# Performance work log

Measured on AMD Instinct MI355X. Metric: run time of the kernel, lower is better.

The kernel has to match this reference:

```python
import jax, jax.numpy as jnp
import numpy as np

B, T, NG, NP, DV = 256, 100, 4096, 512, 2


def setup_inputs() -> dict:
    key = jax.random.key(0)
    k = jax.random.split(key, 6)
    v = jax.random.normal(k[0], (B, T, DV), dtype=jnp.float32) * 0.1
    P0 = jax.random.uniform(k[1], (B, NP), dtype=jnp.float32)
    # Dense kernels (glorot-ish scale); recurrent kernel uniform(-0.02, 0.02) per the module
    W_enc = jax.random.normal(k[2], (NP, NG), dtype=jnp.float32) / np.sqrt(NP)
    W_in = jax.random.normal(k[3], (DV, NG), dtype=jnp.float32) / np.sqrt(DV)
    W_rec = (jax.random.uniform(k[4], (NG, NG), dtype=jnp.float32) * 2.0 - 1.0) * 0.02
    W_dec = jax.random.normal(k[5], (NG, NP), dtype=jnp.float32) / np.sqrt(NG)
    return {"v": v, "P0": P0, "W_enc": W_enc, "W_in": W_in, "W_rec": W_rec, "W_dec": W_dec}


def reference(v, P0, W_enc, W_in, W_rec, W_dec):
    # encoder: init hidden state from place-cell code P0  -> [B, Ng]
    h0 = P0 @ W_enc
    # Precompute input projection for all timesteps: [B, T, Ng] -> scan over T
    xW = jnp.einsum('btd,dg->btg', v, W_in)
    xW_t = jnp.swapaxes(xW, 0, 1)  # [T, B, Ng]

    def step(h, x):
        h_new = jax.nn.relu(x + h @ W_rec)
        return h_new, h_new

    _, g = jax.lax.scan(step, h0, xW_t)      # g: [T, B, Ng]
    g = jnp.swapaxes(g, 0, 1)                # [B, T, Ng]
    place_preds = jnp.einsum('btg,gp->btp', g, W_dec)  # [B, T, Np]
    return place_preds
```

## Files before the change

### kernel.cpp

```cpp
#include <hip/hip_runtime.h>
#include <hip/hip_bf16.h>

typedef __attribute__((ext_vector_type(8))) short bf16x8;
typedef __attribute__((ext_vector_type(4))) float f32x4;

#define MFMA __builtin_amdgcn_mfma_f32_16x16x32_bf16

__device__ __forceinline__ short f2bf(float f) {
    union { __hip_bfloat16 h; short s; } u;
    u.h = __float2bfloat16(f);
    return u.s;
}

__device__ __forceinline__ void gld_lds16(const void* g, void* l) {
    auto gp = (const __attribute__((address_space(1))) void*)(g);
    auto lp = (__attribute__((address_space(3))) void*)(l);
    __builtin_amdgcn_global_load_lds(gp, lp, 16, 0, 0);
}

__global__ __launch_bounds__(64) void cvt_tile(const float* __restrict__ in,
                                               __hip_bfloat16* __restrict__ out, int C) {
    const int cd32 = C >> 5;
    const int tile = blockIdx.x;
    const int r16 = tile / cd32, c32 = tile - r16 * cd32;
    const int l = threadIdx.x;
    const int row = (r16 << 4) + (l & 15);
    const int c0 = (c32 << 5) + ((l >> 4) << 3);
    const float* src = in + (size_t)row * C + c0;
    short o[8];
#pragma unroll
    for (int j = 0; j < 8; ++j) o[j] = f2bf(src[j]);
    *(bf16x8*)((char*)out + (size_t)tile * 1024 + (l << 4)) = *(bf16x8*)o;
}

__global__ __launch_bounds__(64) void tcvt_tile(const float* __restrict__ in,
                                                __hip_bfloat16* __restrict__ out,
                                                int N, int K) {
    const int kd32 = K >> 5;
    const int tile = blockIdx.x;
    const int n16 = tile / kd32, k32 = tile - n16 * kd32;
    const int l = threadIdx.x;
    const int n = (n16 << 4) + (l & 15);
    const int k0 = (k32 << 5) + ((l >> 4) << 3);
    short o[8];
#pragma unroll
    for (int j = 0; j < 8; ++j) o[j] = f2bf(in[(size_t)(k0 + j) * N + n]);
    *(bf16x8*)((char*)out + (size_t)tile * 1024 + (l << 4)) = *(bf16x8*)o;
}

template <int MODE, int KC>
__global__ __launch_bounds__(256, 1) void gemm_w(const __hip_bfloat16* __restrict__ A,
                                                 const __hip_bfloat16* __restrict__ B,
                                                 void* __restrict__ outp,
                                                 const float* __restrict__ v,
                                                 const float* __restrict__ Wi, int t) {
    constexpr int KD32 = KC * 4;
    __shared__ __align__(16) char lds[131072];
    const int id = blockIdx.x;
    int bm, bn;
    if constexpr (MODE == 2) {
        int xcd = id & 7, idx = id >> 3;
        int sw = xcd * 400 + idx;
        bm = sw >> 3;
        bn = sw & 7;
    } else {
        int xcd = id & 7, j = id >> 3;
        bn = (xcd << 3) + (j & 7);
        bm = j >> 3;
    }
    const int tid = threadIdx.x, wv = tid >> 6, lane = tid & 63;
    char* myl = lds + (wv << 15);
    const int kw0 = wv * KC;
    const int bm4 = bm << 2, bn4 = bn << 2;

    f32x4 acc[4][4] = {};

    auto stage = [&](int s) {
        char* dst = myl + ((s & 3) << 13);
#pragma unroll
        for (int f = 0; f < 4; ++f) {
            gld_lds16((const char*)A + ((size_t)((bm4 + f) * KD32 + kw0 + s) << 10) + (lane << 4),
                      dst + (f << 10));
            gld_lds16((const char*)B + ((size_t)((bn4 + f) * KD32 + kw0 + s) << 10) + (lane << 4),
                      dst + 4096 + (f << 10));
        }
    };

#define KSTEP(S, DOST)                                                       \
    {                                                                        \
        const char* buf_ = myl + (((S) & 3) << 13);                          \
        bf16x8 a_[4], b_[4];                                                 \
        _Pragma("unroll") for (int f = 0; f < 4; ++f) {                      \
            a_[f] = *(const bf16x8*)(buf_ + (f << 10) + (lane << 4));        \
            b_[f] = *(const bf16x8*)(buf_ + 4096 + (f << 10) + (lane << 4)); \
        }                                                                    \
        if (DOST) stage((S) + 3);                                            \
        _Pragma("unroll") for (int f = 0; f < 4; ++f)                        \
            _Pragma("unroll") for (int g = 0; g < 4; ++g)                    \
                acc[f][g] = MFMA(a_[f], b_[g], acc[f][g], 0, 0, 0);          \
    }

    stage(0);
    __builtin_amdgcn_sched_barrier(0);
    stage(1);
    __builtin_amdgcn_sched_barrier(0);
    stage(2);
    __builtin_amdgcn_sched_barrier(0);

    for (int s = 0; s < KC - 2; ++s) {
        asm volatile("s_waitcnt vmcnt(16)" ::: "memory");
        __builtin_amdgcn_sched_barrier(0);
        KSTEP(s, s + 3 < KC);
    }
    asm volatile("s_waitcnt vmcnt(8)" ::: "memory");
    __builtin_amdgcn_sched_barrier(0);
    KSTEP(KC - 2, false);
    asm volatile("s_waitcnt vmcnt(0)" ::: "memory");
    __builtin_amdgcn_sched_barrier(0);
    KSTEP(KC - 1, false);
#undef KSTEP

    __syncthreads();
#pragma unroll
    for (int f = 0; f < 4; ++f)
#pragma unroll
        for (int g = 0; g < 4; ++g)
            *(f32x4*)(lds + (wv << 14) + (((f << 2) + g) << 10) + (lane << 4)) = acc[f][g];
    __syncthreads();
    f32x4 fin[4];
#pragma unroll
    for (int g = 0; g < 4; ++g) {
        f32x4 s0 = *(const f32x4*)(lds + (0 << 14) + ((((wv << 2) + g)) << 10) + (lane << 4));
        f32x4 s1 = *(const f32x4*)(lds + (1 << 14) + ((((wv << 2) + g)) << 10) + (lane << 4));
        f32x4 s2 = *(const f32x4*)(lds + (2 << 14) + ((((wv << 2) + g)) << 10) + (lane << 4));
        f32x4 s3 = *(const f32x4*)(lds + (3 << 14) + ((((wv << 2) + g)) << 10) + (lane << 4));
        fin[g] = (s0 + s1) + (s2 + s3);
    }

    const int rbase = (bm << 6) + (wv << 4) + ((lane >> 4) << 2);
    const int cbase = (bn << 6) + (lane & 15);

    if constexpr (MODE == 0 || MODE == 1) {
        char* O = (char*)outp;
#pragma unroll
        for (int j = 0; j < 4; ++j) {
            int r = rbase + j;
            float v0 = 0.f, v1 = 0.f;
            if constexpr (MODE == 1) {
                v0 = v[(size_t)(r * 100 + t) * 2 + 0];
                v1 = v[(size_t)(r * 100 + t) * 2 + 1];
            }
#pragma unroll
            for (int g = 0; g < 4; ++g) {
                int c = cbase + (g << 4);
                float val = fin[g][j];
                if constexpr (MODE == 1) {
                    val = fmaxf(val + v0 * Wi[c] + v1 * Wi[4096 + c], 0.0f);
                }
                size_t off = ((size_t)(r >> 4) * 128 + (c >> 5)) * 1024 +
                             ((size_t)((r & 15) + (((c >> 3) & 3) << 4)) << 4) +
                             ((c & 7) << 1);
                *(short*)(O + off) = f2bf(val);
            }
        }
    } else {
        float* O = (float*)outp;
#pragma unroll
        for (int j = 0; j < 4; ++j) {
            int r = rbase + j;
            int tt = r >> 8;
            int b = r & 255;
#pragma unroll
            for (int g = 0; g < 4; ++g) {
                int c = cbase + (g << 4);
                O[((size_t)b * 100 + tt) * 512 + c] = fin[g][j];
            }
        }
    }
}

extern "C" void kernel_launch(void* const* d_in, const int* in_sizes, int n_in,
                              void* d_out, int out_size, void* d_ws, size_t ws_size,
                              hipStream_t stream) {
    const float* v     = (const float*)d_in[0];
    const float* P0    = (const float*)d_in[1];
    const float* W_enc = (const float*)d_in[2];
    const float* W_in  = (const float*)d_in[3];
    const float* W_rec = (const float*)d_in[4];
    const float* W_dec = (const float*)d_in[5];
    float* out = (float*)d_out;

    char* ws = (char*)d_ws;
    __hip_bfloat16* Wrt = (__hip_bfloat16*)(ws + 0);
    __hip_bfloat16* Wet = (__hip_bfloat16*)(ws + 33554432);
    __hip_bfloat16* Wdt = (__hip_bfloat16*)(ws + 37748736);
    __hip_bfloat16* P0t = (__hip_bfloat16*)(ws + 41943040);
    __hip_bfloat16* h0  = (__hip_bfloat16*)(ws + 42205184);
    __hip_bfloat16* G   = (__hip_bfloat16*)(ws + 44302336);

    tcvt_tile<<<32768, 64, 0, stream>>>(W_rec, Wrt, 4096, 4096);
    tcvt_tile<<<4096, 64, 0, stream>>>(W_enc, Wet, 4096, 512);
    tcvt_tile<<<4096, 64, 0, stream>>>(W_dec, Wdt, 512, 4096);
    cvt_tile<<<256, 64, 0, stream>>>(P0, P0t, 512);

    gemm_w<0, 4><<<256, 256, 0, stream>>>(P0t, Wet, (void*)h0, nullptr, nullptr, 0);

    for (int t = 0; t < 100; ++t) {
        const __hip_bfloat16* hprev = (t == 0) ? h0 : (G + (size_t)(t - 1) * 1048576);
        gemm_w<1, 32><<<256, 256, 0, stream>>>(hprev, Wrt,
                                               (void*)(G + (size_t)t * 1048576), v, W_in, t);
    }

    gemm_w<2, 32><<<3200, 256, 0, stream>>>(G, Wdt, (void*)out, nullptr, nullptr, 0);
}
```

Baseline: 1.639 ms.

## Load A fragments directly to registers, stage only B through LDS, halve LDS

The GEMM now stages only the B operand through LDS with global_load_lds. The A operand goes straight from global memory into registers across four rotating register sets, and the k-loop is unrolled by four with static slot indices. Per-wave LDS drops from 32KB to 16KB, so the block uses 64KB and the launch-bounds minimum of one block per SM is removed, which could allow two blocks per CU. The aim is to cut LDS traffic and round trips, but it raises VGPR pressure, and the vmcnt accounting now has to cover register loads mixed with LDS-direct loads.

```diff
diff --git a/kernel.cpp b/kernel.cpp
--- a/kernel.cpp
+++ b/kernel.cpp
@@ -49,13 +49,13 @@
 }
 
 template <int MODE, int KC>
-__global__ __launch_bounds__(256, 1) void gemm_w(const __hip_bfloat16* __restrict__ A,
-                                                 const __hip_bfloat16* __restrict__ B,
-                                                 void* __restrict__ outp,
-                                                 const float* __restrict__ v,
-                                                 const float* __restrict__ Wi, int t) {
+__global__ __launch_bounds__(256) void gemm_w(const __hip_bfloat16* __restrict__ A,
+                                              const __hip_bfloat16* __restrict__ B,
+                                              void* __restrict__ outp,
+                                              const float* __restrict__ v,
+                                              const float* __restrict__ Wi, int t) {
     constexpr int KD32 = KC * 4;
-    __shared__ __align__(16) char lds[131072];
+    __shared__ __align__(16) char lds[65536];
     const int id = blockIdx.x;
     int bm, bn;
     if constexpr (MODE == 2) {
@@ -69,71 +69,111 @@
         bm = j >> 3;
     }
     const int tid = threadIdx.x, wv = tid >> 6, lane = tid & 63;
-    char* myl = lds + (wv << 15);
+    char* myl = lds + (wv << 14);
     const int kw0 = wv * KC;
     const int bm4 = bm << 2, bn4 = bn << 2;
 
+    constexpr size_t FSTR = (size_t)KD32 << 10;
+    const char* pA = (const char*)A + (((size_t)(bm4 * KD32 + kw0)) << 10) + (lane << 4);
+    const char* pB = (const char*)B + (((size_t)(bn4 * KD32 + kw0)) << 10) + (lane << 4);
+
     f32x4 acc[4][4] = {};
-
-    auto stage = [&](int s) {
-        char* dst = myl + ((s & 3) << 13);
-#pragma unroll
-        for (int f = 0; f < 4; ++f) {
-            gld_lds16((const char*)A + ((size_t)((bm4 + f) * KD32 + kw0 + s) << 10) + (lane << 4),
-                      dst + (f << 10));
-            gld_lds16((const char*)B + ((size_t)((bn4 + f) * KD32 + kw0 + s) << 10) + (lane << 4),
-                      dst + 4096 + (f << 10));
-        }
-    };
-
-#define KSTEP(S, DOST)                                                       \
-    {                                                                        \
-        const char* buf_ = myl + (((S) & 3) << 13);                          \
-        bf16x8 a_[4], b_[4];                                                 \
-        _Pragma("unroll") for (int f = 0; f < 4; ++f) {                      \
-            a_[f] = *(const bf16x8*)(buf_ + (f << 10) + (lane << 4));        \
-            b_[f] = *(const bf16x8*)(buf_ + 4096 + (f << 10) + (lane << 4)); \
-        }                                                                    \
-        if (DOST) stage((S) + 3);                                            \
-        _Pragma("unroll") for (int f = 0; f < 4; ++f)                        \
-            _Pragma("unroll") for (int g = 0; g < 4; ++g)                    \
-                acc[f][g] = MFMA(a_[f], b_[g], acc[f][g], 0, 0, 0);          \
-    }
-
-    stage(0);
+    bf16x8 A00, A01, A02, A03, A10, A11, A12, A13,
+           A20, A21, A22, A23, A30, A31, A32, A33;
+
+#define STAGEB(SLOT, KI)                                   \
+    do {                                                   \
+        const char* pb_ = pB + ((size_t)(KI) << 10);       \
+        char* d_ = myl + ((SLOT) << 12);                   \
+        gld_lds16(pb_, d_);                                \
+        gld_lds16(pb_ + FSTR, d_ + 1024);                  \
+        gld_lds16(pb_ + 2 * FSTR, d_ + 2048);              \
+        gld_lds16(pb_ + 3 * FSTR, d_ + 3072);              \
+    } while (0)
+
+#define LOADA(S, KI)                                       \
+    do {                                                   \
+        const char* pa_ = pA + ((size_t)(KI) << 10);       \
+        A##S##0 = *(const bf16x8*)(pa_);                   \
+        A##S##1 = *(const bf16x8*)(pa_ + FSTR);            \
+        A##S##2 = *(const bf16x8*)(pa_ + 2 * FSTR);        \
+        A##S##3 = *(const bf16x8*)(pa_ + 3 * FSTR);        \
+    } while (0)
+
+#define COMPUTE(S)                                                    \
+    do {                                                              \
+        const char* bb_ = myl + ((S) << 12) + (lane << 4);            \
+        bf16x8 b0 = *(const bf16x8*)(bb_);                            \
+        bf16x8 b1 = *(const bf16x8*)(bb_ + 1024);                     \
+        bf16x8 b2 = *(const bf16x8*)(bb_ + 2048);                     \
+        bf16x8 b3 = *(const bf16x8*)(bb_ + 3072);                     \
+        acc[0][0] = MFMA(A##S##0, b0, acc[0][0], 0, 0, 0);            \
+        acc[0][1] = MFMA(A##S##0, b1, acc[0][1], 0, 0, 0);            \
+        acc[0][2] = MFMA(A##S##0, b2, acc[0][2], 0, 0, 0);            \
+        acc[0][3] = MFMA(A##S##0, b3, acc[0][3], 0, 0, 0);            \
+        acc[1][0] = MFMA(A##S##1, b0, acc[1][0], 0, 0, 0);            \
+        acc[1][1] = MFMA(A##S##1, b1, acc[1][1], 0, 0, 0);            \
+        acc[1][2] = MFMA(A##S##1, b2, acc[1][2], 0, 0, 0);            \
+        acc[1][3] = MFMA(A##S##1, b3, acc[1][3], 0, 0, 0);            \
+        acc[2][0] = MFMA(A##S##2, b0, acc[2][0], 0, 0, 0);            \
+        acc[2][1] = MFMA(A##S##2, b1, acc[2][1], 0, 0, 0);            \
+        acc[2][2] = MFMA(A##S##2, b2, acc[2][2], 0, 0, 0);            \
+        acc[2][3] = MFMA(A##S##2, b3, acc[2][3], 0, 0, 0);            \
+        acc[3][0] = MFMA(A##S##3, b0, acc[3][0], 0, 0, 0);            \
+        acc[3][1] = MFMA(A##S##3, b1, acc[3][1], 0, 0, 0);            \
+        acc[3][2] = MFMA(A##S##3, b2, acc[3][2], 0, 0, 0);            \
+        acc[3][3] = MFMA(A##S##3, b3, acc[3][3], 0, 0, 0);            \
+    } while (0)
+
+#define ITER(S, SP, VM, DOISS, KI)                                 \
+    do {                                                           \
+        asm volatile("s_waitcnt vmcnt(%0)" ::"i"(VM) : "memory");  \
+        __builtin_amdgcn_sched_barrier(0);                         \
+        if (DOISS) {                                               \
+            STAGEB(SP, (KI) + 3);                                  \
+            LOADA(SP, (KI) + 3);                                   \
+        }                                                          \
+        __builtin_amdgcn_sched_barrier(0);                         \
+        COMPUTE(S);                                                \
+    } while (0)
+
+    STAGEB(0, 0); LOADA(0, 0);
     __builtin_amdgcn_sched_barrier(0);
-    stage(1);
+    STAGEB(1, 1); LOADA(1, 1);
     __builtin_amdgcn_sched_barrier(0);
-    stage(2);
+    STAGEB(2, 2); LOADA(2, 2);
     __builtin_amdgcn_sched_barrier(0);
 
-    for (int s = 0; s < KC - 2; ++s) {
-        asm volatile("s_waitcnt vmcnt(16)" ::: "memory");
-        __builtin_amdgcn_sched_barrier(0);
-        KSTEP(s, s + 3 < KC);
-    }
-    asm volatile("s_waitcnt vmcnt(8)" ::: "memory");
-    __builtin_amdgcn_sched_barrier(0);
-    KSTEP(KC - 2, false);
-    asm volatile("s_waitcnt vmcnt(0)" ::: "memory");
-    __builtin_amdgcn_sched_barrier(0);
-    KSTEP(KC - 1, false);
-#undef KSTEP
-
-    __syncthreads();
+    int s = 0;
+    for (; s + 4 < KC; s += 4) {
+        ITER(0, 3, 16, true, s + 0);
+        ITER(1, 0, 16, true, s + 1);
+        ITER(2, 1, 16, true, s + 2);
+        ITER(3, 2, 16, true, s + 3);
+    }
+    ITER(0, 3, 16, true,  s + 0);
+    ITER(1, 0, 16, false, s + 1);
+    ITER(2, 1, 8,  false, s + 2);
+    ITER(3, 2, 0,  false, s + 3);
+
+#undef ITER
+#undef COMPUTE
+#undef LOADA
+#undef STAGEB
+
 #pragma unroll
     for (int f = 0; f < 4; ++f)
 #pragma unroll
         for (int g = 0; g < 4; ++g)
-            *(f32x4*)(lds + (wv << 14) + (((f << 2) + g) << 10) + (lane << 4)) = acc[f][g];
+            *(f32x4*)(myl + (((f << 2) + g) << 10) + (lane << 4)) = acc[f][g];
     __syncthreads();
     f32x4 fin[4];
 #pragma unroll
     for (int g = 0; g < 4; ++g) {
-        f32x4 s0 = *(const f32x4*)(lds + (0 << 14) + ((((wv << 2) + g)) << 10) + (lane << 4));
-        f32x4 s1 = *(const f32x4*)(lds + (1 << 14) + ((((wv << 2) + g)) << 10) + (lane << 4));
-        f32x4 s2 = *(const f32x4*)(lds + (2 << 14) + ((((wv << 2) + g)) << 10) + (lane << 4));
-        f32x4 s3 = *(const f32x4*)(lds + (3 << 14) + ((((wv << 2) + g)) << 10) + (lane << 4));
+        f32x4 s0 = *(const f32x4*)(lds + (0 << 14) + (((wv << 2) + g) << 10) + (lane << 4));
+        f32x4 s1 = *(const f32x4*)(lds + (1 << 14) + (((wv << 2) + g) << 10) + (lane << 4));
+        f32x4 s2 = *(const f32x4*)(lds + (2 << 14) + (((wv << 2) + g) << 10) + (lane << 4));
+        f32x4 s3 = *(const f32x4*)(lds + (3 << 14) + (((wv << 2) + g) << 10) + (lane << 4));
         fin[g] = (s0 + s1) + (s2 + s3);
     }
 
```

Measured after the change: 1.707 ms. 1.04x slower.
